# Optimization experiments

Measured on AMD Instinct MI355X. Metric: run time of the kernel, lower is better.

The kernel has to match this reference:

```python
import jax, jax.numpy as jnp
import numpy as np
import math

D_MODEL = 1024
N_HEADS = 16
D_HEAD = D_MODEL // N_HEADS
LSR_RANK = 32
B, T = 4, 2048


def setup_inputs() -> dict:
    key = jax.random.key(0)
    ks = jax.random.split(key, 11)
    s = 1.0 / math.sqrt(D_MODEL)
    x = jax.random.normal(ks[0], (B, T, D_MODEL), dtype=jnp.float32)
    Wq = jax.random.uniform(ks[1], (D_MODEL, D_MODEL), minval=-s, maxval=s)
    bq = jax.random.uniform(ks[2], (D_MODEL,), minval=-s, maxval=s)
    Wk = jax.random.uniform(ks[3], (D_MODEL, D_MODEL), minval=-s, maxval=s)
    bk = jax.random.uniform(ks[4], (D_MODEL,), minval=-s, maxval=s)
    Wv = jax.random.uniform(ks[5], (D_MODEL, D_MODEL), minval=-s, maxval=s)
    bv = jax.random.uniform(ks[6], (D_MODEL,), minval=-s, maxval=s)
    Wo = jax.random.uniform(ks[7], (D_MODEL, D_MODEL), minval=-s, maxval=s)
    bo = jax.random.uniform(ks[8], (D_MODEL,), minval=-s, maxval=s)
    Wq_lsr = jax.random.normal(ks[9], (N_HEADS, D_HEAD, LSR_RANK)) / math.sqrt(D_HEAD)
    Wk_lsr = jax.random.normal(ks[10], (N_HEADS, D_HEAD, LSR_RANK)) / math.sqrt(D_HEAD)
    return {"x": x, "Wq": Wq, "bq": bq, "Wk": Wk, "bk": bk,
            "Wv": Wv, "bv": bv, "Wo": Wo, "bo": bo,
            "Wq_lsr": Wq_lsr, "Wk_lsr": Wk_lsr}


def reference(x, Wq, bq, Wk, bk, Wv, bv, Wo, bo, Wq_lsr, Wk_lsr):
    Bq, Tq, _ = x.shape
    # Linear projections (torch Linear: x @ W.T + b), split into heads -> (B,H,T,Dh)
    def split_heads(y):
        return y.reshape(Bq, Tq, N_HEADS, D_HEAD).transpose(0, 2, 1, 3)
    q = split_heads(x @ Wq.T + bq)
    k = split_heads(x @ Wk.T + bk)
    v = split_heads(x @ Wv.T + bv)
    # LSR: project q,k to rank-R per head
    q_lr = jnp.einsum('bhtd,hdr->bhtr', q, Wq_lsr)
    k_lr = jnp.einsum('bhtd,hdr->bhtr', k, Wk_lsr)
    scale = 1.0 / math.sqrt(max(LSR_RANK, 1))
    scores = jnp.einsum('bhir,bhjr->bhij', q_lr, k_lr) * scale  # (B,H,T,T)
    causal_mask = jnp.triu(jnp.ones((Tq, Tq), dtype=bool), k=1)
    scores = jnp.where(causal_mask, jnp.float32(-jnp.inf), scores)
    attn = jax.nn.softmax(scores, axis=-1)
    y = jnp.einsum('bhij,bhjd->bhid', attn, v)  # (B,H,T,Dh)
    y = y.transpose(0, 2, 1, 3).reshape(Bq, Tq, D_MODEL)
    return y @ Wo.T + bo
```

## Files before the change

kernel.cpp:

```cpp
#include <hip/hip_runtime.h>

#define B_  4
#define T_  2048
#define H_  16
#define DM_ 1024
#define DH_ 64
#define RK_ 32

using u16 = unsigned short;
using u32 = unsigned int;
typedef float  floatx4 __attribute__((ext_vector_type(4)));
typedef __bf16 bf16x8  __attribute__((ext_vector_type(8)));
typedef u16    u16x8   __attribute__((ext_vector_type(8)));
typedef u16    u16x4   __attribute__((ext_vector_type(4)));
typedef short  s16x4   __attribute__((ext_vector_type(4)));

#define MFMA16(a,b,c) __builtin_amdgcn_mfma_f32_16x16x32_bf16((a),(b),(c),0,0,0)
#define MFMA1K(a,b,c) __builtin_amdgcn_mfma_f32_16x16x16bf16_1k((a),(b),(c),0,0,0)

__device__ __forceinline__ u16 f2bf(float f) {
  unsigned u = __float_as_uint(f);
  u += 0x7fffu + ((u >> 16) & 1u);
  return (u16)(u >> 16);
}
__device__ __forceinline__ float b2f(u16 h) {
  return __uint_as_float(((unsigned)h) << 16);
}
__device__ __forceinline__ u32 pack_bf(float a, float b) {
  u32 ua = __float_as_uint(a); ua += 0x7fffu + ((ua >> 16) & 1u);
  u32 ub = __float_as_uint(b); ub += 0x7fffu + ((ub >> 16) & 1u);
  return __builtin_amdgcn_perm(ub, ua, 0x07060302u);
}
__device__ __forceinline__ u32 tpack(float a, float b) {
  return __builtin_amdgcn_perm(__float_as_uint(b), __float_as_uint(a), 0x07060302u);
}

__device__ __forceinline__ void async_copy16(const u16* g, const u16* lds_uniform_base) {
  __builtin_amdgcn_global_load_lds(
      (const __attribute__((address_space(1))) unsigned int*)(unsigned long long)g,
      (__attribute__((address_space(3))) unsigned int*)(unsigned int)(unsigned long long)lds_uniform_base,
      16, 0, 0);
}

__global__ __launch_bounds__(256) void cvt_x(const float* __restrict__ s,
                                             u16* __restrict__ d, int n4) {
  int i = blockIdx.x * 256 + threadIdx.x;
  if (i >= n4) return;
  float4 v = reinterpret_cast<const float4*>(s)[i];
  u16x4 o = { f2bf(v.x), f2bf(v.y), f2bf(v.z), f2bf(v.w) };
  reinterpret_cast<u16x4*>(d)[i] = o;
}

__global__ __launch_bounds__(256) void cvt_weights(const float* __restrict__ Wq,
                                                   const float* __restrict__ Wk,
                                                   const float* __restrict__ Wv,
                                                   const float* __restrict__ Wo,
                                                   u16* __restrict__ Wcat) {
  int i = blockIdx.x * 256 + threadIdx.x;
  int reg = i >> 18;
  const float* s = (reg == 0) ? Wq : (reg == 1) ? Wk : (reg == 2) ? Wv : Wo;
  int j = i & 262143;
  float4 v = reinterpret_cast<const float4*>(s)[j];
  u16x4 o = { f2bf(v.x), f2bf(v.y), f2bf(v.z), f2bf(v.w) };
  reinterpret_cast<u16x4*>(Wcat)[i] = o;
}

template <int OUTF32>
__global__ __launch_bounds__(256, 2) void gemm8(const u16* __restrict__ A,
                                                const u16* __restrict__ W,
                                                const float* __restrict__ b0,
                                                const float* __restrict__ b1,
                                                const float* __restrict__ b2,
                                                void* __restrict__ Cv, int ldc) {
  __shared__ __align__(16) u16 Al[2][8192];
  __shared__ __align__(16) u16 Bl[2][8192];
  const int tid  = threadIdx.x;
  const int lane = tid & 63;
  const int w    = tid >> 6;
  const int quad = lane >> 4;
  const int l16  = lane & 15;
  const int wm   = (w >> 1) << 6;
  const int wn   = (w & 1) << 6;

  const int bm = blockIdx.x << 7;
  const int bn = blockIdx.y << 7;

  const int sr = tid >> 3;
  const int sc = ((tid & 7) ^ (sr & 7)) * 8;
  const u16* Ag = A + (size_t)(bm + sr) * 1024 + sc;
  const u16* Wg = W + (size_t)(bn + sr) * 1024 + sc;

  auto stage = [&](int k0, int bsel) {
#pragma unroll
    for (int j = 0; j < 4; j++)
      async_copy16(Ag + (size_t)j * 32768 + k0, &Al[bsel][j * 2048 + w * 512]);
#pragma unroll
    for (int j = 0; j < 4; j++)
      async_copy16(Wg + (size_t)j * 32768 + k0, &Bl[bsel][j * 2048 + w * 512]);
  };

  int aoff[4], boff[4], sl[2];
#pragma unroll
  for (int mi = 0; mi < 4; mi++) aoff[mi] = (wm + mi * 16 + l16) * 64;
#pragma unroll
  for (int ni = 0; ni < 4; ni++) boff[ni] = (wn + ni * 16 + l16) * 64;
  sl[0] = ((0 + quad) ^ (l16 & 7)) * 8;
  sl[1] = ((4 + quad) ^ (l16 & 7)) * 8;

  floatx4 acc[4][4];
#pragma unroll
  for (int i = 0; i < 4; i++)
#pragma unroll
    for (int j = 0; j < 4; j++) acc[i][j] = (floatx4){0.f, 0.f, 0.f, 0.f};

  stage(0, 0);
  asm volatile("s_waitcnt vmcnt(0)" ::: "memory");
  __builtin_amdgcn_s_barrier();
  asm volatile("" ::: "memory");

  for (int i = 0; i < 16; i++) {
    if (i < 15) stage((i + 1) * 64, (i + 1) & 1);
    const u16* Ab = Al[i & 1];
    const u16* Bb = Bl[i & 1];
#pragma unroll
    for (int ks = 0; ks < 2; ks++) {
      bf16x8 af[4], bfr[4];
#pragma unroll
      for (int mi = 0; mi < 4; mi++)
        af[mi] = *reinterpret_cast<const bf16x8*>(Ab + aoff[mi] + sl[ks]);
#pragma unroll
      for (int ni = 0; ni < 4; ni++)
        bfr[ni] = *reinterpret_cast<const bf16x8*>(Bb + boff[ni] + sl[ks]);
      __builtin_amdgcn_s_setprio(1);
#pragma unroll
      for (int mi = 0; mi < 4; mi++)
#pragma unroll
        for (int ni = 0; ni < 4; ni++)
          acc[mi][ni] = MFMA16(af[mi], bfr[ni], acc[mi][ni]);
      __builtin_amdgcn_s_setprio(0);
    }
    if (i < 15) {
      asm volatile("s_waitcnt vmcnt(0)" ::: "memory");
      __builtin_amdgcn_s_barrier();
      asm volatile("" ::: "memory");
    }
  }

  const float* bp = (bn < 1024) ? b0 : ((bn < 2048) ? b1 : b2);
#pragma unroll
  for (int ni = 0; ni < 4; ni++) {
    int col = bn + wn + ni * 16 + l16;
    float bias = bp[col & 1023];
#pragma unroll
    for (int mi = 0; mi < 4; mi++)
#pragma unroll
      for (int r = 0; r < 4; r++) {
        int row = bm + wm + mi * 16 + quad * 4 + r;
        float v = acc[mi][ni][r] + bias;
        if (OUTF32)
          reinterpret_cast<float*>(Cv)[(size_t)row * ldc + col] = v;
        else
          reinterpret_cast<u16*>(Cv)[(size_t)row * ldc + col] = f2bf(v);
      }
  }
}

__global__ __launch_bounds__(256) void vtrans(const u16* __restrict__ qkv,
                                              u16* __restrict__ vt) {
  const int tb = blockIdx.x;
  const int bh = blockIdx.y;
  const int b = bh >> 4, h = bh & 15;
  __shared__ u16 Vl[64][72];
  const int tid = threadIdx.x;
#pragma unroll
  for (int it = 0; it < 2; it++) {
    int c = it * 256 + tid;
    int t = c >> 3, dc = (c & 7) * 8;
    u16x8 v = *reinterpret_cast<const u16x8*>(
        qkv + (size_t)(b * T_ + tb * 64 + t) * 3072 + 2048 + h * 64 + dc);
    *reinterpret_cast<u16x8*>(&Vl[t][dc]) = v;
  }
  __syncthreads();
#pragma unroll
  for (int it = 0; it < 2; it++) {
    int c = it * 256 + tid;
    int d = c >> 3, tt = (c & 7) * 8;
    u16x8 o;
#pragma unroll
    for (int j = 0; j < 8; j++) o[j] = Vl[tt + j][d];
    *reinterpret_cast<u16x8*>(vt + ((size_t)bh * 64 + d) * T_ + tb * 64 + tt) = o;
  }
}

__global__ __launch_bounds__(256) void lsr_mfma(const u16* __restrict__ qkv,
                                                const float* __restrict__ Wql,
                                                const float* __restrict__ Wkl,
                                                u16* __restrict__ qlr,
                                                u16* __restrict__ klr) {
  const int t0 = blockIdx.x * 128;
  const int bh = blockIdx.y, b = bh >> 4, h = bh & 15;
  const int sel = blockIdx.z;
  const int tid = threadIdx.x, lane = tid & 63, w = tid >> 6;
  const int quad = lane >> 4, l16 = lane & 15;
  __shared__ __align__(16) u16 Al[128 * 64];
  __shared__ __align__(16) u16 Wl[32 * 72];

  const float* Wsrc = (sel ? Wkl : Wql) + h * 2048;
  const float fold = sel ? 1.0f : 0.25506100790944405f;
  {
    float4 a = *reinterpret_cast<const float4*>(Wsrc + tid * 8);
    float4 c = *reinterpret_cast<const float4*>(Wsrc + tid * 8 + 4);
    float vals[8] = {a.x, a.y, a.z, a.w, c.x, c.y, c.z, c.w};
#pragma unroll
    for (int i = 0; i < 8; i++) {
      int idx = tid * 8 + i, d = idx >> 5, r = idx & 31;
      Wl[r * 72 + d] = f2bf(vals[i] * fold);
    }
  }
#pragma unroll
  for (int issue = 0; issue < 4; issue++) {
    int l = issue * 256 + tid;
    int t = l >> 3, ck = l & 7;
    const u16* src = qkv + (size_t)(b * T_ + t0 + t) * 3072 + sel * 1024 + h * 64 +
                     ((ck ^ (t & 7)) * 8);
    async_copy16(src, Al + issue * 2048 + w * 512);
  }
  __syncthreads();

  bf16x8 wf[2][2], af[2][2];
#pragma unroll
  for (int mr = 0; mr < 2; mr++)
#pragma unroll
    for (int c = 0; c < 2; c++)
      wf[mr][c] = *reinterpret_cast<const bf16x8*>(&Wl[(mr * 16 + l16) * 72 + c * 32 + quad * 8]);
#pragma unroll
  for (int i = 0; i < 2; i++) {
    int t = (2 * w + i) * 16 + l16;
#pragma unroll
    for (int c = 0; c < 2; c++)
      af[i][c] = *reinterpret_cast<const bf16x8*>(&Al[t * 64 + (((4 * c + quad) ^ (t & 7)) * 8)]);
  }
  floatx4 acc[2][2];
#pragma unroll
  for (int i = 0; i < 2; i++)
#pragma unroll
    for (int mr = 0; mr < 2; mr++) acc[i][mr] = (floatx4){0.f, 0.f, 0.f, 0.f};
#pragma unroll
  for (int i = 0; i < 2; i++)
#pragma unroll
    for (int mr = 0; mr < 2; mr++)
#pragma unroll
      for (int c = 0; c < 2; c++)
        acc[i][mr] = MFMA16(wf[mr][c], af[i][c], acc[i][mr]);

  u16* outp = sel ? klr : qlr;
#pragma unroll
  for (int i = 0; i < 2; i++) {
    int t = t0 + (2 * w + i) * 16 + l16;
#pragma unroll
    for (int mr = 0; mr < 2; mr++) {
      uint2 pv = { pack_bf(acc[i][mr][0], acc[i][mr][1]),
                   pack_bf(acc[i][mr][2], acc[i][mr][3]) };
      *reinterpret_cast<uint2*>(outp + ((size_t)bh * T_ + t) * 32 + mr * 16 + quad * 4) = pv;
    }
  }
}

__global__ __launch_bounds__(256, 4) void attn(const u16* __restrict__ qlr,
                                               const u16* __restrict__ klr,
                                               const u16* __restrict__ vt,
                                               u16* __restrict__ yatt) {
  const int bh = blockIdx.y;
  const int b = bh >> 4, h = bh & 15;
  const int p = blockIdx.x;
  const int tid = threadIdx.x, lane = tid & 63, w = tid >> 6;
  const int quad = lane >> 4, l16 = lane & 15;

  __shared__ __align__(16) u16 Vt3[3][4096];
  __shared__ __align__(16) u16 Kt3[3][2048];

  const u16* qlr_bh = qlr + (size_t)bh * T_ * RK_;
  const u16* klr_bh = klr + (size_t)bh * T_ * RK_;
  const u16* vt_bh  = vt + (size_t)bh * 64 * T_;

  int voff[4][4];
#pragma unroll
  for (int nt = 0; nt < 4; nt++)
#pragma unroll
    for (int dt = 0; dt < 4; dt++) {
      int d = dt * 16 + l16;
      voff[nt][dt] = d * 64 + (((nt * 2 + (quad >> 1)) ^ (d & 7)) * 8) + (quad & 1) * 4;
    }
  int soffV[2];
#pragma unroll
  for (int issue = 0; issue < 2; issue++) {
    int L = issue * 256 + tid;
    int d = L >> 3, cg = L & 7;
    soffV[issue] = d * T_ + ((cg ^ (d & 7)) * 8);
  }
  const int soffK = (w * 8 + (lane >> 3)) * 64 + (((lane & 7) ^ (lane >> 3)) * 8);
  const int koff = (l16 >> 1) * 64 + ((((l16 & 1) * 4 + quad) ^ (l16 >> 1)) * 8);
  const int wub = w * 512;

  const floatx4 fzero = {0.f, 0.f, 0.f, 0.f};

  for (int run = 0; run < 2; run++) {
    const int qi = run ? p : 31 - p;
    const int q0 = qi * 64;
    if (run) __syncthreads();

    bf16x8 qf = *reinterpret_cast<const bf16x8*>(
        qlr_bh + (size_t)(q0 + w * 16 + l16) * 32 + quad * 8);

    auto stage = [&](int t, int bi) {
      const u16* vs = vt_bh + t * 64;
      async_copy16(vs + soffV[0], &Vt3[bi][wub]);
      async_copy16(vs + soffV[1], &Vt3[bi][2048 + wub]);
      async_copy16(klr_bh + t * 2048 + soffK, &Kt3[bi][wub]);
    };

    stage(0, 0);
    if (qi >= 1) {
      stage(1, 1);
      asm volatile("s_waitcnt vmcnt(3)" ::: "memory");
    } else {
      asm volatile("s_waitcnt vmcnt(0)" ::: "memory");
    }
    __builtin_amdgcn_s_barrier();
    asm volatile("" ::: "memory");

    floatx4 oacc[4];
#pragma unroll
    for (int i = 0; i < 4; i++) oacc[i] = fzero;
    float rs = 0.f;

    const u16* Vb = &Vt3[0][0];
    const u16* Kb = &Kt3[0][0];
    int cb = 0, sb = 2;

    for (int i = 0; i < qi; i++) {
      const bool do_stage = (i + 2 <= qi);
      if (do_stage) stage(i + 2, sb);

      bf16x8 kf[4];
#pragma unroll
      for (int nt = 0; nt < 4; nt++)
        kf[nt] = *reinterpret_cast<const bf16x8*>(Kb + koff + nt * 512);
      floatx4 sv[4];
#pragma unroll
      for (int nt = 0; nt < 4; nt++) sv[nt] = MFMA16(kf[nt], qf, fzero);

      uint2 pk[4];
#pragma unroll
      for (int nt = 0; nt < 4; nt++) {
        float p0 = __builtin_amdgcn_exp2f(sv[nt][0]);
        float p1 = __builtin_amdgcn_exp2f(sv[nt][1]);
        float p2 = __builtin_amdgcn_exp2f(sv[nt][2]);
        float p3 = __builtin_amdgcn_exp2f(sv[nt][3]);
        rs += (p0 + p1) + (p2 + p3);
        pk[nt].x = tpack(p0, p1);
        pk[nt].y = tpack(p2, p3);
      }
#pragma unroll
      for (int dt = 0; dt < 4; dt++)
#pragma unroll
        for (int nt = 0; nt < 4; nt++) {
          s16x4 vf = *reinterpret_cast<const s16x4*>(Vb + voff[nt][dt]);
          oacc[dt] = MFMA1K(vf, __builtin_bit_cast(s16x4, pk[nt]), oacc[dt]);
        }

      if (do_stage) asm volatile("s_waitcnt vmcnt(3)" ::: "memory");
      else          asm volatile("s_waitcnt vmcnt(0)" ::: "memory");
      __builtin_amdgcn_s_barrier();
      asm volatile("" ::: "memory");

      cb = (cb == 2) ? 0 : cb + 1;
      Vb = &Vt3[cb][0];
      Kb = &Kt3[cb][0];
      if (do_stage) sb = (sb == 2) ? 0 : sb + 1;
    }

    {
      bf16x8 kf[4];
#pragma unroll
      for (int nt = 0; nt < 4; nt++)
        kf[nt] = *reinterpret_cast<const bf16x8*>(Kb + koff + nt * 512);
      floatx4 sv[4];
#pragma unroll
      for (int nt = 0; nt < 4; nt++) sv[nt] = MFMA16(kf[nt], qf, fzero);
      const int thr = w * 16 + l16;
      uint2 pk[4];
#pragma unroll
      for (int nt = 0; nt < 4; nt++) {
        float pr[4];
#pragma unroll
        for (int r = 0; r < 4; r++) {
          float e = __builtin_amdgcn_exp2f(sv[nt][r]);
          pr[r] = (nt * 16 + quad * 4 + r <= thr) ? e : 0.f;
        }
        rs += (pr[0] + pr[1]) + (pr[2] + pr[3]);
        pk[nt].x = tpack(pr[0], pr[1]);
        pk[nt].y = tpack(pr[2], pr[3]);
      }
#pragma unroll
      for (int dt = 0; dt < 4; dt++)
#pragma unroll
        for (int nt = 0; nt < 4; nt++) {
          s16x4 vf = *reinterpret_cast<const s16x4*>(Vb + voff[nt][dt]);
          oacc[dt] = MFMA1K(vf, __builtin_bit_cast(s16x4, pk[nt]), oacc[dt]);
        }
    }

    rs += __shfl_xor(rs, 16);
    rs += __shfl_xor(rs, 32);
    float inv = 1.f / rs;
    const int qrow = q0 + w * 16 + l16;
#pragma unroll
    for (int dt = 0; dt < 4; dt++) {
      uint2 ov = { pack_bf(oacc[dt][0] * inv, oacc[dt][1] * inv),
                   pack_bf(oacc[dt][2] * inv, oacc[dt][3] * inv) };
      *reinterpret_cast<uint2*>(
          yatt + (size_t)(b * T_ + qrow) * 1024 + h * 64 + dt * 16 + quad * 4) = ov;
    }
  }
}

extern "C" void kernel_launch(void* const* d_in, const int* in_sizes, int n_in,
                              void* d_out, int out_size, void* d_ws, size_t ws_size,
                              hipStream_t stream) {
  const float* x   = (const float*)d_in[0];
  const float* Wq  = (const float*)d_in[1];
  const float* bq  = (const float*)d_in[2];
  const float* Wk  = (const float*)d_in[3];
  const float* bk  = (const float*)d_in[4];
  const float* Wv  = (const float*)d_in[5];
  const float* bv  = (const float*)d_in[6];
  const float* Wo  = (const float*)d_in[7];
  const float* bo  = (const float*)d_in[8];
  const float* Wql = (const float*)d_in[9];
  const float* Wkl = (const float*)d_in[10];
  float* out = (float*)d_out;

  char* ws = (char*)d_ws;
  u16* xb   = (u16*)(ws);
  u16* Wcat = (u16*)(ws + 16777216);
  u16* qkv  = (u16*)(ws + 25165824);
  u16* qlr  = (u16*)(ws + 75497472);
  u16* klr  = (u16*)(ws + 83886080);
  u16* yatt = (u16*)(ws + 92274688);
  u16* vt   = xb;

  cvt_x<<<dim3(8192), 256, 0, stream>>>(x, xb, 2097152);
  cvt_weights<<<dim3(4096), 256, 0, stream>>>(Wq, Wk, Wv, Wo, Wcat);
  gemm8<0><<<dim3(64, 24), 256, 0, stream>>>(xb, Wcat, bq, bk, bv, qkv, 3072);
  vtrans<<<dim3(32, 64), 256, 0, stream>>>(qkv, vt);
  lsr_mfma<<<dim3(16, 64, 2), 256, 0, stream>>>(qkv, Wql, Wkl, qlr, klr);
  attn<<<dim3(16, 64), 256, 0, stream>>>(qlr, klr, vt, yatt);
  gemm8<1><<<dim3(64, 8), 256, 0, stream>>>(yatt, Wcat + 3145728, bo, bo, bo, out, 1024);
}
```

Before: 253.3 us.

## Fold LSR projections into Q/K weights and shrink the QKV GEMM

Precomputes effective weights Wq·Wq_lsr and Wk·Wk_lsr (with biases) on device, so the input GEMM produces V plus rank-32 q/k directly. This removes the separate LSR kernel, the full-width q/k intermediates, and a third of the projection GEMM work. It adds two small fold kernels per call and rounds the folded weights to bf16, which slightly changes numerics. The new epilogue writes q_lr/k_lr with a scattered per-element layout.

```diff
diff --git a/kernel.cpp b/kernel.cpp
--- a/kernel.cpp
+++ b/kernel.cpp
@@ -23,9 +23,6 @@
   u += 0x7fffu + ((u >> 16) & 1u);
   return (u16)(u >> 16);
 }
-__device__ __forceinline__ float b2f(u16 h) {
-  return __uint_as_float(((unsigned)h) << 16);
-}
 __device__ __forceinline__ u32 pack_bf(float a, float b) {
   u32 ua = __float_as_uint(a); ua += 0x7fffu + ((ua >> 16) & 1u);
   u32 ub = __float_as_uint(b); ub += 0x7fffu + ((ub >> 16) & 1u);
@@ -51,27 +48,55 @@
   reinterpret_cast<u16x4*>(d)[i] = o;
 }
 
-__global__ __launch_bounds__(256) void cvt_weights(const float* __restrict__ Wq,
-                                                   const float* __restrict__ Wk,
-                                                   const float* __restrict__ Wv,
-                                                   const float* __restrict__ Wo,
-                                                   u16* __restrict__ Wcat) {
+__global__ __launch_bounds__(256) void cvt_wvo(const float* __restrict__ Wv,
+                                               const float* __restrict__ Wo,
+                                               u16* __restrict__ Wcat) {
   int i = blockIdx.x * 256 + threadIdx.x;
   int reg = i >> 18;
-  const float* s = (reg == 0) ? Wq : (reg == 1) ? Wk : (reg == 2) ? Wv : Wo;
+  const float* s = reg ? Wo : Wv;
   int j = i & 262143;
   float4 v = reinterpret_cast<const float4*>(s)[j];
   u16x4 o = { f2bf(v.x), f2bf(v.y), f2bf(v.z), f2bf(v.w) };
-  reinterpret_cast<u16x4*>(Wcat)[i] = o;
-}
-
-template <int OUTF32>
+  reinterpret_cast<u16x4*>(Wcat)[(reg ? 524288 : 0) + j] = o;
+}
+
+__global__ __launch_bounds__(256) void lsr_fold(const float* __restrict__ W,
+                                                const float* __restrict__ bias,
+                                                const float* __restrict__ lsr,
+                                                float fold,
+                                                u16* __restrict__ Weff,
+                                                float* __restrict__ beff) {
+  const int hr = blockIdx.x;
+  const int h = hr >> 5, r = hr & 31;
+  const int tid = threadIdx.x;
+  __shared__ float lw[64];
+  if (tid < 64) lw[tid] = lsr[(size_t)(h * 64 + tid) * 32 + r] * fold;
+  __syncthreads();
+  float a0 = 0.f, a1 = 0.f, a2 = 0.f, a3 = 0.f;
+  for (int d = 0; d < 64; d++) {
+    float l = lw[d];
+    float4 wv = *reinterpret_cast<const float4*>(W + (size_t)(h * 64 + d) * 1024 + tid * 4);
+    a0 += l * wv.x; a1 += l * wv.y; a2 += l * wv.z; a3 += l * wv.w;
+  }
+  u16x4 o = { f2bf(a0), f2bf(a1), f2bf(a2), f2bf(a3) };
+  reinterpret_cast<u16x4*>(Weff)[(size_t)hr * 256 + tid] = o;
+  if (tid == 0) {
+    float s = 0.f;
+    for (int d = 0; d < 64; d++) s += lw[d] * bias[h * 64 + d];
+    beff[hr] = s;
+  }
+}
+
+template <int MODE>
 __global__ __launch_bounds__(256, 2) void gemm8(const u16* __restrict__ A,
                                                 const u16* __restrict__ W,
                                                 const float* __restrict__ b0,
                                                 const float* __restrict__ b1,
                                                 const float* __restrict__ b2,
-                                                void* __restrict__ Cv, int ldc) {
+                                                void* __restrict__ Cv,
+                                                u16* __restrict__ qo,
+                                                u16* __restrict__ ko,
+                                                int ldc) {
   __shared__ __align__(16) u16 Al[2][8192];
   __shared__ __align__(16) u16 Bl[2][8192];
   const int tid  = threadIdx.x;
@@ -146,26 +171,57 @@
     }
   }
 
-  const float* bp = (bn < 1024) ? b0 : ((bn < 2048) ? b1 : b2);
-#pragma unroll
-  for (int ni = 0; ni < 4; ni++) {
-    int col = bn + wn + ni * 16 + l16;
-    float bias = bp[col & 1023];
-#pragma unroll
-    for (int mi = 0; mi < 4; mi++)
-#pragma unroll
-      for (int r = 0; r < 4; r++) {
-        int row = bm + wm + mi * 16 + quad * 4 + r;
-        float v = acc[mi][ni][r] + bias;
-        if (OUTF32)
-          reinterpret_cast<float*>(Cv)[(size_t)row * ldc + col] = v;
-        else
-          reinterpret_cast<u16*>(Cv)[(size_t)row * ldc + col] = f2bf(v);
+  if (MODE == 1) {
+#pragma unroll
+    for (int ni = 0; ni < 4; ni++) {
+      int col = bn + wn + ni * 16 + l16;
+      float bias = b0[col & 1023];
+#pragma unroll
+      for (int mi = 0; mi < 4; mi++)
+#pragma unroll
+        for (int r = 0; r < 4; r++) {
+          int row = bm + wm + mi * 16 + quad * 4 + r;
+          reinterpret_cast<float*>(Cv)[(size_t)row * ldc + col] = acc[mi][ni][r] + bias;
+        }
+    }
+  } else {
+    if (bn < 1024) {
+#pragma unroll
+      for (int ni = 0; ni < 4; ni++) {
+        int col = bn + wn + ni * 16 + l16;
+        float bias = b0[col];
+#pragma unroll
+        for (int mi = 0; mi < 4; mi++)
+#pragma unroll
+          for (int r = 0; r < 4; r++) {
+            int row = bm + wm + mi * 16 + quad * 4 + r;
+            reinterpret_cast<u16*>(Cv)[(size_t)row * 1024 + col] =
+                f2bf(acc[mi][ni][r] + bias);
+          }
       }
-  }
-}
-
-__global__ __launch_bounds__(256) void vtrans(const u16* __restrict__ qkv,
+    } else {
+      u16* outp = (bn < 1536) ? qo : ko;
+      const float* bp = (bn < 1536) ? b1 : b2;
+#pragma unroll
+      for (int ni = 0; ni < 4; ni++) {
+        int cc = (bn + wn + ni * 16 + l16) & 511;
+        float bias = bp[cc];
+        int hh = cc >> 5, rk = cc & 31;
+#pragma unroll
+        for (int mi = 0; mi < 4; mi++)
+#pragma unroll
+          for (int r = 0; r < 4; r++) {
+            int row = bm + wm + mi * 16 + quad * 4 + r;
+            size_t addr =
+                ((size_t)((row >> 11) * 16 + hh) * 2048 + (row & 2047)) * 32 + rk;
+            outp[addr] = f2bf(acc[mi][ni][r] + bias);
+          }
+      }
+    }
+  }
+}
+
+__global__ __launch_bounds__(256) void vtrans(const u16* __restrict__ V,
                                               u16* __restrict__ vt) {
   const int tb = blockIdx.x;
   const int bh = blockIdx.y;
@@ -177,7 +233,7 @@
     int c = it * 256 + tid;
     int t = c >> 3, dc = (c & 7) * 8;
     u16x8 v = *reinterpret_cast<const u16x8*>(
-        qkv + (size_t)(b * T_ + tb * 64 + t) * 3072 + 2048 + h * 64 + dc);
+        V + (size_t)(b * T_ + tb * 64 + t) * 1024 + h * 64 + dc);
     *reinterpret_cast<u16x8*>(&Vl[t][dc]) = v;
   }
   __syncthreads();
@@ -189,80 +245,6 @@
 #pragma unroll
     for (int j = 0; j < 8; j++) o[j] = Vl[tt + j][d];
     *reinterpret_cast<u16x8*>(vt + ((size_t)bh * 64 + d) * T_ + tb * 64 + tt) = o;
-  }
-}
-
-__global__ __launch_bounds__(256) void lsr_mfma(const u16* __restrict__ qkv,
-                                                const float* __restrict__ Wql,
-                                                const float* __restrict__ Wkl,
-                                                u16* __restrict__ qlr,
-                                                u16* __restrict__ klr) {
-  const int t0 = blockIdx.x * 128;
-  const int bh = blockIdx.y, b = bh >> 4, h = bh & 15;
-  const int sel = blockIdx.z;
-  const int tid = threadIdx.x, lane = tid & 63, w = tid >> 6;
-  const int quad = lane >> 4, l16 = lane & 15;
-  __shared__ __align__(16) u16 Al[128 * 64];
-  __shared__ __align__(16) u16 Wl[32 * 72];
-
-  const float* Wsrc = (sel ? Wkl : Wql) + h * 2048;
-  const float fold = sel ? 1.0f : 0.25506100790944405f;
-  {
-    float4 a = *reinterpret_cast<const float4*>(Wsrc + tid * 8);
-    float4 c = *reinterpret_cast<const float4*>(Wsrc + tid * 8 + 4);
-    float vals[8] = {a.x, a.y, a.z, a.w, c.x, c.y, c.z, c.w};
-#pragma unroll
-    for (int i = 0; i < 8; i++) {
-      int idx = tid * 8 + i, d = idx >> 5, r = idx & 31;
-      Wl[r * 72 + d] = f2bf(vals[i] * fold);
-    }
-  }
-#pragma unroll
-  for (int issue = 0; issue < 4; issue++) {
-    int l = issue * 256 + tid;
-    int t = l >> 3, ck = l & 7;
-    const u16* src = qkv + (size_t)(b * T_ + t0 + t) * 3072 + sel * 1024 + h * 64 +
-                     ((ck ^ (t & 7)) * 8);
-    async_copy16(src, Al + issue * 2048 + w * 512);
-  }
-  __syncthreads();
-
-  bf16x8 wf[2][2], af[2][2];
-#pragma unroll
-  for (int mr = 0; mr < 2; mr++)
-#pragma unroll
-    for (int c = 0; c < 2; c++)
-      wf[mr][c] = *reinterpret_cast<const bf16x8*>(&Wl[(mr * 16 + l16) * 72 + c * 32 + quad * 8]);
-#pragma unroll
-  for (int i = 0; i < 2; i++) {
-    int t = (2 * w + i) * 16 + l16;
-#pragma unroll
-    for (int c = 0; c < 2; c++)
-      af[i][c] = *reinterpret_cast<const bf16x8*>(&Al[t * 64 + (((4 * c + quad) ^ (t & 7)) * 8)]);
-  }
-  floatx4 acc[2][2];
-#pragma unroll
-  for (int i = 0; i < 2; i++)
-#pragma unroll
-    for (int mr = 0; mr < 2; mr++) acc[i][mr] = (floatx4){0.f, 0.f, 0.f, 0.f};
-#pragma unroll
-  for (int i = 0; i < 2; i++)
-#pragma unroll
-    for (int mr = 0; mr < 2; mr++)
-#pragma unroll
-      for (int c = 0; c < 2; c++)
-        acc[i][mr] = MFMA16(wf[mr][c], af[i][c], acc[i][mr]);
-
-  u16* outp = sel ? klr : qlr;
-#pragma unroll
-  for (int i = 0; i < 2; i++) {
-    int t = t0 + (2 * w + i) * 16 + l16;
-#pragma unroll
-    for (int mr = 0; mr < 2; mr++) {
-      uint2 pv = { pack_bf(acc[i][mr][0], acc[i][mr][1]),
-                   pack_bf(acc[i][mr][2], acc[i][mr][3]) };
-      *reinterpret_cast<uint2*>(outp + ((size_t)bh * T_ + t) * 32 + mr * 16 + quad * 4) = pv;
-    }
   }
 }
 
@@ -442,19 +424,26 @@
   float* out = (float*)d_out;
 
   char* ws = (char*)d_ws;
-  u16* xb   = (u16*)(ws);
-  u16* Wcat = (u16*)(ws + 16777216);
-  u16* qkv  = (u16*)(ws + 25165824);
-  u16* qlr  = (u16*)(ws + 75497472);
-  u16* klr  = (u16*)(ws + 83886080);
-  u16* yatt = (u16*)(ws + 92274688);
-  u16* vt   = xb;
+  u16*   xb    = (u16*)(ws);
+  u16*   Wcat  = (u16*)(ws + 16777216);
+  float* beffq = (float*)(ws + 23068672);
+  float* beffk = (float*)(ws + 23072768);
+  u16*   Vbuf  = (u16*)(ws + 25165824);
+  u16*   qlr   = (u16*)(ws + 41943040);
+  u16*   klr   = (u16*)(ws + 50331648);
+  u16*   yatt  = (u16*)(ws + 58720256);
+  u16*   vt    = xb;
+
+  const float foldq = 0.25506100790944405f;
 
   cvt_x<<<dim3(8192), 256, 0, stream>>>(x, xb, 2097152);
-  cvt_weights<<<dim3(4096), 256, 0, stream>>>(Wq, Wk, Wv, Wo, Wcat);
-  gemm8<0><<<dim3(64, 24), 256, 0, stream>>>(xb, Wcat, bq, bk, bv, qkv, 3072);
-  vtrans<<<dim3(32, 64), 256, 0, stream>>>(qkv, vt);
-  lsr_mfma<<<dim3(16, 64, 2), 256, 0, stream>>>(qkv, Wql, Wkl, qlr, klr);
+  cvt_wvo<<<dim3(2048), 256, 0, stream>>>(Wv, Wo, Wcat);
+  lsr_fold<<<dim3(512), 256, 0, stream>>>(Wq, bq, Wql, foldq, Wcat + 1048576, beffq);
+  lsr_fold<<<dim3(512), 256, 0, stream>>>(Wk, bk, Wkl, 1.0f, Wcat + 1572864, beffk);
+  gemm8<2><<<dim3(64, 16), 256, 0, stream>>>(xb, Wcat, bv, beffq, beffk,
+                                             Vbuf, qlr, klr, 0);
+  vtrans<<<dim3(32, 64), 256, 0, stream>>>(Vbuf, vt);
   attn<<<dim3(16, 64), 256, 0, stream>>>(qlr, klr, vt, yatt);
-  gemm8<1><<<dim3(64, 8), 256, 0, stream>>>(yatt, Wcat + 3145728, bo, bo, bo, out, 1024);
-}
+  gemm8<1><<<dim3(64, 8), 256, 0, stream>>>(yatt, Wcat + 2097152, bo, bo, bo,
+                                            out, nullptr, nullptr, 1024);
+}
```

After: 241.3 us. -4.7%, faster.
